# Kernel tuning notes

Measured on AMD Instinct MI355X. Metric: run time of the kernel, lower is better.

Reference implementation:

```python
import jax, jax.numpy as jnp
import numpy as np

N = 50000      # num_nodes
E = 300000     # edges per edge type
T = 3          # num_edge_type
C = 2          # num_channels
F_IN = 64      # feature_size
HID = 64       # hidden_size (w_out)
NL = 2         # num_layers (GT layers per FastGTN)
BETA = 0.5     # gtn_beta
TP = 0.8       # teleport_probability


def setup_inputs() -> dict:
    key = jax.random.key(0)
    ks = jax.random.split(key, 16)
    X = jax.random.normal(ks[0], (N, F_IN), dtype=jnp.float32)
    edge_index_0 = jax.random.randint(ks[1], (2, E), 0, N)
    edge_index_1 = jax.random.randint(ks[2], (2, E), 0, N)
    edge_index_2 = jax.random.randint(ks[3], (2, E), 0, N)
    edge_value_0 = jax.random.uniform(ks[4], (E,), dtype=jnp.float32)
    edge_value_1 = jax.random.uniform(ks[5], (E,), dtype=jnp.float32)
    edge_value_2 = jax.random.uniform(ks[6], (E,), dtype=jnp.float32)
    # glorot for Ws (per-channel projection), std=0.1 for GT layer mixing weights
    g0 = np.sqrt(6.0 / (F_IN + HID))
    g1 = np.sqrt(6.0 / (HID + HID))
    Ws0 = jax.random.uniform(ks[7], (C, F_IN, HID), minval=-g0, maxval=g0, dtype=jnp.float32)
    Ws1 = jax.random.uniform(ks[8], (C, HID, HID), minval=-g1, maxval=g1, dtype=jnp.float32)
    layerW0 = 0.1 * jax.random.normal(ks[9], (NL, C, T), dtype=jnp.float32)
    layerW1 = 0.1 * jax.random.normal(ks[10], (NL, C, T), dtype=jnp.float32)
    gl = np.sqrt(1.0 / (C * HID))
    lin_W0 = jax.random.uniform(ks[11], (C * HID, HID), minval=-gl, maxval=gl, dtype=jnp.float32)
    lin_b0 = jax.random.uniform(ks[12], (HID,), minval=-gl, maxval=gl, dtype=jnp.float32)
    lin_W1 = jax.random.uniform(ks[13], (C * HID, HID), minval=-gl, maxval=gl, dtype=jnp.float32)
    lin_b1 = jax.random.uniform(ks[14], (HID,), minval=-gl, maxval=gl, dtype=jnp.float32)
    return dict(X=X,
                edge_value_0=edge_value_0, edge_value_1=edge_value_1, edge_value_2=edge_value_2,
                Ws0=Ws0, Ws1=Ws1, layerW0=layerW0, layerW1=layerW1,
                lin_W0=lin_W0, lin_b0=lin_b0, lin_W1=lin_W1, lin_b1=lin_b1,
                edge_index_0=edge_index_0, edge_index_1=edge_index_1, edge_index_2=edge_index_2)


def _spmm_mix(H, filt, vals, etype, row, col):
    # H: [C, N, d]; filt: [C, T] softmaxed; vals: [Etot]; etype/row/col: [Etot]
    # == for each channel c: sum_j filt[c,j] * (A_j @ H[c])
    w = vals[None, :] * filt[:, etype]          # [C, Etot]
    msg = w[:, :, None] * H[:, col, :]          # [C, Etot, d]
    return jax.vmap(lambda m: jax.ops.segment_sum(m, row, num_segments=N))(msg)


def _fastgtn_block(Xin, Ws, layerW, linW, linb, row, col, vals, etype):
    H = jnp.einsum('nf,cfo->cno', Xin, Ws)      # [C, N, HID]
    X0 = jax.lax.stop_gradient(H)               # X_ = H.clone().detach()
    for l in range(NL):
        filt = jax.nn.softmax(layerW[l], axis=1)
        H = _spmm_mix(H, filt, vals, etype, row, col)
    Hm = TP * jax.nn.relu(BETA * X0 + (1.0 - BETA) * H) + (1.0 - TP) * X0
    Hm = jnp.transpose(Hm, (1, 0, 2)).reshape(N, C * Hm.shape[-1])  # [N, C*HID]
    return jax.nn.relu(Hm @ linW + linb)


def reference(X, edge_value_0, edge_value_1, edge_value_2,
              Ws0, Ws1, layerW0, layerW1,
              lin_W0, lin_b0, lin_W1, lin_b1,
              edge_index_0, edge_index_1, edge_index_2):
    row = jnp.concatenate([edge_index_0[0], edge_index_1[0], edge_index_2[0]])
    col = jnp.concatenate([edge_index_0[1], edge_index_1[1], edge_index_2[1]])
    vals = jnp.concatenate([edge_value_0, edge_value_1, edge_value_2])
    etype = jnp.repeat(jnp.arange(T), E)
    H = _fastgtn_block(X, Ws0, layerW0, lin_W0, lin_b0, row, col, vals, etype)
    H = _fastgtn_block(H, Ws1, layerW1, lin_W1, lin_b1, row, col, vals, etype)
    return H
```

## Files before the change

### kernel.cpp

```cpp
#include <hip/hip_runtime.h>
#include <hip/hip_fp16.h>

#define NN 50000
#define EE 300000
#define ETOT (3 * EE)
#define HD 64
#define RB 256
#define NB 196
#define CHUNK 8192
#define NBLKT ((EE + CHUNK - 1) / CHUNK)
#define NBT (3 * NBLKT)
#define NTOT (NB * NBT)
#define GS_VPT ((NTOT + 1023) / 1024)
#define MAXB 6144
#define PROJ_NTILE (NN / 16)
#define PP_GRID (NBT + 512)


__global__ void __launch_bounds__(256)
hist1_kernel(const int* __restrict__ ei0, const int* __restrict__ ei1,
             const int* __restrict__ ei2, int* __restrict__ hist) {
    __shared__ int lh[NB];
    int t = blockIdx.y;
    const int* ei = (t == 0) ? ei0 : (t == 1) ? ei1 : ei2;
    int tid = threadIdx.x;
    for (int i = tid; i < NB; i += 256) lh[i] = 0;
    __syncthreads();
    int e0 = blockIdx.x * CHUNK;
    for (int it = 0; it < CHUNK / 256; ++it) {
        int e = e0 + it * 256 + tid;
        if (e < EE) atomicAdd(&lh[ei[e] >> 8], 1);
    }
    __syncthreads();
    int flat = t * NBLKT + blockIdx.x;
    for (int i = tid; i < NB; i += 256) hist[flat * NB + i] = lh[i];
}

__global__ void __launch_bounds__(1024)
gscan_kernel(const int* __restrict__ hist, int* __restrict__ gbase,
             int* __restrict__ bbase, int* __restrict__ rp,
             const float* __restrict__ lw0, const float* __restrict__ lw1,
             float* __restrict__ filt) {
    __shared__ int wsum[16];
    int tid = threadIdx.x, lane = tid & 63, wv = tid >> 6;
    if (tid < 8) {
        int b = tid >> 2, l = (tid >> 1) & 1, c = tid & 1;
        const float* lw = (b == 0 ? lw0 : lw1) + l * 6 + c * 3;
        float a0 = lw[0], a1 = lw[1], a2 = lw[2];
        float m  = fmaxf(a0, fmaxf(a1, a2));
        float e0 = expf(a0 - m), e1 = expf(a1 - m), e2 = expf(a2 - m);
        float s  = e0 + e1 + e2;
        float* o = filt + tid * 3;
        o[0] = e0 / s; o[1] = e1 / s; o[2] = e2 / s;
    }
    int s0 = tid * GS_VPT;
    int local = 0;
    for (int j = 0; j < GS_VPT; ++j) {
        int s = s0 + j;
        if (s < NTOT) {
            int bucket = s / NBT, flat = s - bucket * NBT;
            local += hist[flat * NB + bucket];
        }
    }
    int x = local;
#pragma unroll
    for (int d = 1; d < 64; d <<= 1) {
        int y = __shfl_up(x, d);
        if (lane >= d) x += y;
    }
    if (lane == 63) wsum[wv] = x;
    __syncthreads();
    if (tid == 0) {
        int s = 0;
        for (int i = 0; i < 16; ++i) { int t = wsum[i]; wsum[i] = s; s += t; }
    }
    __syncthreads();
    int run = x + wsum[wv] - local;
    for (int j = 0; j < GS_VPT; ++j) {
        int s = s0 + j;
        if (s < NTOT) {
            int bucket = s / NBT, flat = s - bucket * NBT;
            gbase[flat * NB + bucket] = run;
            if (flat == 0) bbase[bucket] = run;
            run += hist[flat * NB + bucket];
        }
    }
    if (tid == 0) { bbase[NB] = ETOT; rp[NN] = ETOT; }
}

__global__ void __launch_bounds__(256)
place_proj_kernel(const int* __restrict__ ei0, const int* __restrict__ ei1,
                  const int* __restrict__ ei2,
                  const float* __restrict__ ev0, const float* __restrict__ ev1,
                  const float* __restrict__ ev2,
                  const int* __restrict__ gbase, uint2* __restrict__ staged,
                  const float* __restrict__ Xin, const float* __restrict__ Ws,
                  __half2* __restrict__ Hh) {
    __shared__ float Wl[2 * 64 * 64];
    __shared__ float Xs[16 * 65];
    __shared__ int   lbase[NB];
    int tid = threadIdx.x;

    if (blockIdx.x < NBT) {
        int flat = blockIdx.x;
        int t  = flat / NBLKT;
        int bx = flat - t * NBLKT;
        const int*   ei = (t == 0) ? ei0 : (t == 1) ? ei1 : ei2;
        const float* ev = (t == 0) ? ev0 : (t == 1) ? ev1 : ev2;
        for (int i = tid; i < NB; i += 256) lbase[i] = gbase[flat * NB + i];
        __syncthreads();
        int e0 = bx * CHUNK;
        for (int it = 0; it < CHUNK / 256; ++it) {
            int e = e0 + it * 256 + tid;
            if (e < EE) {
                int row = ei[e];
                int col = ei[EE + e];
                unsigned int q = (unsigned int)__float2int_rn(ev[e] * 16383.0f);
                unsigned int mw = (unsigned int)col | ((unsigned int)t << 16) | (q << 18);
                int pos = atomicAdd(&lbase[row >> 8], 1);
                staged[pos] = make_uint2(mw, (unsigned int)row);
            }
        }
    } else {
        for (int i = tid; i < 2 * 64 * 64; i += 256) Wl[i] = Ws[i];
        int oq = (tid & 15) * 4;
        int ln = tid >> 4;
        for (int tile = blockIdx.x - NBT; tile < PROJ_NTILE; tile += 512) {
            int n0 = tile * 16;
            __syncthreads();
            for (int i = tid; i < 16 * 64; i += 256)
                Xs[(i >> 6) * 65 + (i & 63)] = Xin[(n0 + (i >> 6)) * 64 + (i & 63)];
            __syncthreads();
            float a0[4] = {0.f, 0.f, 0.f, 0.f};
            float a1[4] = {0.f, 0.f, 0.f, 0.f};
            for (int f = 0; f < 64; ++f) {
                float  x  = Xs[ln * 65 + f];
                float4 w0 = *(const float4*)&Wl[f * 64 + oq];
                float4 w1 = *(const float4*)&Wl[4096 + f * 64 + oq];
                a0[0] += x * w0.x; a0[1] += x * w0.y;
                a0[2] += x * w0.z; a0[3] += x * w0.w;
                a1[0] += x * w1.x; a1[1] += x * w1.y;
                a1[2] += x * w1.z; a1[3] += x * w1.w;
            }
            float4 o4;
            ((__half2*)&o4)[0] = __floats2half2_rn(a0[0], a1[0]);
            ((__half2*)&o4)[1] = __floats2half2_rn(a0[1], a1[1]);
            ((__half2*)&o4)[2] = __floats2half2_rn(a0[2], a1[2]);
            ((__half2*)&o4)[3] = __floats2half2_rn(a0[3], a1[3]);
            *(float4*)&Hh[(n0 + ln) * HD + oq] = o4;
        }
    }
}

__global__ void __launch_bounds__(256)
csr_kernel(const uint2* __restrict__ staged, const int* __restrict__ bbase,
           int* __restrict__ rp, unsigned int* __restrict__ meta) {
    __shared__ int hist[RB];
    __shared__ int lcur[RB];
    __shared__ int wsum[4];
    __shared__ unsigned int metaL[MAXB];
    int b   = blockIdx.x;
    int tid = threadIdx.x;
    int base = bbase[b];
    int cnt  = bbase[b + 1] - base;
    int row0 = b * RB;

    hist[tid] = 0;
    __syncthreads();
    for (int i = tid; i < cnt; i += 256) {
        uint2 s = staged[base + i];
        atomicAdd(&hist[(int)s.y - row0], 1);
    }
    __syncthreads();
    int lane = tid & 63, wv = tid >> 6;
    int v = hist[tid];
    int x = v;
#pragma unroll
    for (int d = 1; d < 64; d <<= 1) {
        int y = __shfl_up(x, d);
        if (lane >= d) x += y;
    }
    if (lane == 63) wsum[wv] = x;
    __syncthreads();
    if (tid == 0) {
        int s = 0;
        for (int i = 0; i < 4; ++i) { int t = wsum[i]; wsum[i] = s; s += t; }
    }
    __syncthreads();
    int excl = x + wsum[wv] - v;
    lcur[tid] = excl;
    int row = row0 + tid;
    if (row < NN) rp[row] = base + excl;
    __syncthreads();
    for (int i = tid; i < cnt; i += 256) {
        uint2 s = staged[base + i];
        int p = atomicAdd(&lcur[(int)s.y - row0], 1);
        metaL[p] = s.x;
    }
    __syncthreads();
    for (int i = tid; i < cnt; i += 256)
        meta[base + i] = metaL[i];
}

__global__ void __launch_bounds__(256)
proj_kernel(const float* __restrict__ Xin, const float* __restrict__ Ws,
            __half2* __restrict__ Hh) {
    __shared__ float Wl[2 * 64 * 64];
    __shared__ float Xs[16 * 65];
    int tid = threadIdx.x;
    for (int i = tid; i < 2 * 64 * 64; i += 256) Wl[i] = Ws[i];
    int oq = (tid & 15) * 4;
    int ln = tid >> 4;
    for (int tile = blockIdx.x; tile < PROJ_NTILE; tile += gridDim.x) {
        int n0 = tile * 16;
        __syncthreads();
        for (int i = tid; i < 16 * 64; i += 256)
            Xs[(i >> 6) * 65 + (i & 63)] = Xin[(n0 + (i >> 6)) * 64 + (i & 63)];
        __syncthreads();
        float a0[4] = {0.f, 0.f, 0.f, 0.f};
        float a1[4] = {0.f, 0.f, 0.f, 0.f};
        for (int f = 0; f < 64; ++f) {
            float  x  = Xs[ln * 65 + f];
            float4 w0 = *(const float4*)&Wl[f * 64 + oq];
            float4 w1 = *(const float4*)&Wl[4096 + f * 64 + oq];
            a0[0] += x * w0.x; a0[1] += x * w0.y;
            a0[2] += x * w0.z; a0[3] += x * w0.w;
            a1[0] += x * w1.x; a1[1] += x * w1.y;
            a1[2] += x * w1.z; a1[3] += x * w1.w;
        }
        float4 o4;
        ((__half2*)&o4)[0] = __floats2half2_rn(a0[0], a1[0]);
        ((__half2*)&o4)[1] = __floats2half2_rn(a0[1], a1[1]);
        ((__half2*)&o4)[2] = __floats2half2_rn(a0[2], a1[2]);
        ((__half2*)&o4)[3] = __floats2half2_rn(a0[3], a1[3]);
        *(float4*)&Hh[(n0 + ln) * HD + oq] = o4;
    }
}

__global__ void __launch_bounds__(256)
spmm_kernel(const float4* __restrict__ Hin4, float4* __restrict__ Hout4,
            const unsigned int* __restrict__ meta, const int* __restrict__ rp,
            const float* __restrict__ filt ) {
    const int wid  = threadIdx.x >> 6;
    const int lane = threadIdx.x & 63;
    const int g    = lane >> 4;
    const int fq   = lane & 15;
    const int row  = blockIdx.x * 4 + wid;

    const float s = 1.0f / 16383.0f;
    const float F00 = filt[0] * s, F01 = filt[1] * s, F02 = filt[2] * s;
    const float F10 = filt[3] * s, F11 = filt[4] * s, F12 = filt[5] * s;

    float accA[4] = {0.f, 0.f, 0.f, 0.f};
    float accB[4] = {0.f, 0.f, 0.f, 0.f};

    const int beg = rp[row], end = rp[row + 1];
    for (int j0 = beg; j0 < end; j0 += 64) {
        int cnt = min(end - j0, 64);
        unsigned int m = (lane < cnt) ? meta[j0 + lane] : 0u;
        for (int k = 0; k < cnt; k += 8) {
            unsigned int mmA = (unsigned int)__shfl((int)m, k + g);
            unsigned int mmB = (unsigned int)__shfl((int)m, k + 4 + g);
            float4 rA = Hin4[(mmA & 0xffffu) * 16 + fq];
            float4 rB = Hin4[(mmB & 0xffffu) * 16 + fq];
            int   etA = (mmA >> 16) & 3,  etB = (mmB >> 16) & 3;
            float qA  = (float)(mmA >> 18), qB = (float)(mmB >> 18);
            float w0A = qA * ((etA == 0) ? F00 : (etA == 1) ? F01 : F02);
            float w1A = qA * ((etA == 0) ? F10 : (etA == 1) ? F11 : F12);
            float w0B = qB * ((etB == 0) ? F00 : (etB == 1) ? F01 : F02);
            float w1B = qB * ((etB == 0) ? F10 : (etB == 1) ? F11 : F12);
#pragma unroll
            for (int i = 0; i < 4; ++i) {
                float2 xA = __half22float2(((const __half2*)&rA)[i]);
                float2 xB = __half22float2(((const __half2*)&rB)[i]);
                accA[i] += w0A * xA.x + w0B * xB.x;
                accB[i] += w1A * xA.y + w1B * xB.y;
            }
        }
    }
#pragma unroll
    for (int i = 0; i < 4; ++i) {
        accA[i] += __shfl_xor(accA[i], 16); accA[i] += __shfl_xor(accA[i], 32);
        accB[i] += __shfl_xor(accB[i], 16); accB[i] += __shfl_xor(accB[i], 32);
    }
    if (g == 0) {
        float4 o4;
        ((__half2*)&o4)[0] = __floats2half2_rn(accA[0], accB[0]);
        ((__half2*)&o4)[1] = __floats2half2_rn(accA[1], accB[1]);
        ((__half2*)&o4)[2] = __floats2half2_rn(accA[2], accB[2]);
        ((__half2*)&o4)[3] = __floats2half2_rn(accA[3], accB[3]);
        Hout4[row * 16 + fq] = o4;
    }
}

#define EPI_TILE 64
#define HS_STRIDE 132
__global__ void __launch_bounds__(256)
epilogue_kernel(const __half2* __restrict__ X0, const __half2* __restrict__ H,
                const float* __restrict__ linW, const float* __restrict__ linb,
                float* __restrict__ out) {
    __shared__ float Wl[128 * 64];
    __shared__ float Hs[EPI_TILE * HS_STRIDE];
    int tid = threadIdx.x;
    for (int i = tid; i < 128 * 64; i += 256) Wl[i] = linW[i];
    int oq = tid & 15, nq = tid >> 4;
    float bias[4];
#pragma unroll
    for (int i = 0; i < 4; ++i) bias[i] = linb[oq + 16 * i];
    const int ntiles = (NN + EPI_TILE - 1) / EPI_TILE;
    for (int tile = blockIdx.x; tile < ntiles; tile += gridDim.x) {
        int n0 = tile * EPI_TILE;
        __syncthreads();
        for (int i = tid; i < EPI_TILE * 64; i += 256) {
            int ln = i >> 6, d = i & 63;
            int n = n0 + ln;
            float2 x0 = make_float2(0.f, 0.f), h = make_float2(0.f, 0.f);
            if (n < NN) {
                x0 = __half22float2(X0[n * HD + d]);
                h  = __half22float2(H [n * HD + d]);
            }
            float z0 = fmaxf(0.5f * x0.x + 0.5f * h.x, 0.f);
            float z1 = fmaxf(0.5f * x0.y + 0.5f * h.y, 0.f);
            Hs[ln * HS_STRIDE + d]      = 0.8f * z0 + 0.2f * x0.x;
            Hs[ln * HS_STRIDE + 64 + d] = 0.8f * z1 + 0.2f * x0.y;
        }
        __syncthreads();
        float acc[4][4];
#pragma unroll
        for (int j = 0; j < 4; ++j)
#pragma unroll
            for (int i = 0; i < 4; ++i) acc[j][i] = bias[i];
        for (int k = 0; k < 128; k += 4) {
            float4 hq[4];
#pragma unroll
            for (int j = 0; j < 4; ++j)
                hq[j] = *(const float4*)&Hs[(nq + 16 * j) * HS_STRIDE + k];
#pragma unroll
            for (int kk = 0; kk < 4; ++kk) {
                float w[4];
#pragma unroll
                for (int i = 0; i < 4; ++i) w[i] = Wl[(k + kk) * 64 + oq + 16 * i];
#pragma unroll
                for (int j = 0; j < 4; ++j) {
                    float x = (kk == 0) ? hq[j].x : (kk == 1) ? hq[j].y
                             : (kk == 2) ? hq[j].z : hq[j].w;
#pragma unroll
                    for (int i = 0; i < 4; ++i) acc[j][i] += x * w[i];
                }
            }
        }
#pragma unroll
        for (int j = 0; j < 4; ++j) {
            int n = n0 + nq + 16 * j;
            if (n < NN) {
#pragma unroll
                for (int i = 0; i < 4; ++i)
                    out[n * HD + oq + 16 * i] = fmaxf(acc[j][i], 0.f);
            }
        }
    }
}

extern "C" void kernel_launch(void* const* d_in, const int* in_sizes, int n_in,
                              void* d_out, int out_size, void* d_ws, size_t ws_size,
                              hipStream_t stream) {
    const float* X     = (const float*)d_in[0];
    const float* ev0   = (const float*)d_in[1];
    const float* ev1   = (const float*)d_in[2];
    const float* ev2   = (const float*)d_in[3];
    const float* Ws0   = (const float*)d_in[4];
    const float* Ws1   = (const float*)d_in[5];
    const float* lw0   = (const float*)d_in[6];
    const float* lw1   = (const float*)d_in[7];
    const float* linW0 = (const float*)d_in[8];
    const float* linb0 = (const float*)d_in[9];
    const float* linW1 = (const float*)d_in[10];
    const float* linb1 = (const float*)d_in[11];
    const int*   ei0   = (const int*)d_in[12];
    const int*   ei1   = (const int*)d_in[13];
    const int*   ei2   = (const int*)d_in[14];
    float* out = (float*)d_out;

    float* ws = (float*)d_ws;
    __half2* X0h = (__half2*)(ws);
    __half2* Ha  = (__half2*)(ws + 1 * NN * HD);
    __half2* Hb  = (__half2*)(ws + 2 * NN * HD);
    float*   mid = ws + 3 * NN * HD;
    uint2*   staged = (uint2*)mid;
    float*   filt   = ws + 4 * NN * HD;
    int*     hist   = (int*)(filt + 32);
    int*     gbase  = hist + NTOT;
    int*     bbase  = gbase + NTOT;
    int*     rp     = bbase + NB + 4;
    unsigned int* meta = (unsigned int*)(rp + NN + 16);

    dim3 egrid(NBLKT, 3);
    hist1_kernel<<<egrid, 256, 0, stream>>>(ei0, ei1, ei2, hist);
    gscan_kernel<<<1, 1024, 0, stream>>>(hist, gbase, bbase, rp,
                                         lw0, lw1, filt);
    place_proj_kernel<<<PP_GRID, 256, 0, stream>>>(ei0, ei1, ei2,
                                                   ev0, ev1, ev2,
                                                   gbase, staged,
                                                   X, Ws0, X0h);
    csr_kernel<<<NB, 256, 0, stream>>>(staged, bbase, rp, meta);

    spmm_kernel<<<NN / 4, 256, 0, stream>>>((const float4*)X0h, (float4*)Ha,
                                            meta, rp, filt + 0);
    spmm_kernel<<<NN / 4, 256, 0, stream>>>((const float4*)Ha, (float4*)Hb,
                                            meta, rp, filt + 6);
    epilogue_kernel<<<512, 256, 0, stream>>>(X0h, Hb, linW0, linb0, mid);

    proj_kernel<<<512, 256, 0, stream>>>(mid, Ws1, X0h);
    spmm_kernel<<<NN / 4, 256, 0, stream>>>((const float4*)X0h, (float4*)Ha,
                                            meta, rp, filt + 12);
    spmm_kernel<<<NN / 4, 256, 0, stream>>>((const float4*)Ha, (float4*)Hb,
                                            meta, rp, filt + 18);
    epilogue_kernel<<<512, 256, 0, stream>>>(X0h, Hb, linW1, linb1, out);
}
```

Before: 392.8 us.

## Fuse next-block projection into epilogue and unroll SpMM gather to four edges

```diff
diff --git a/kernel.cpp b/kernel.cpp
--- a/kernel.cpp
+++ b/kernel.cpp
@@ -202,38 +202,19 @@
         meta[base + i] = metaL[i];
 }
 
-__global__ void __launch_bounds__(256)
-proj_kernel(const float* __restrict__ Xin, const float* __restrict__ Ws,
-            __half2* __restrict__ Hh) {
-    __shared__ float Wl[2 * 64 * 64];
-    __shared__ float Xs[16 * 65];
-    int tid = threadIdx.x;
-    for (int i = tid; i < 2 * 64 * 64; i += 256) Wl[i] = Ws[i];
-    int oq = (tid & 15) * 4;
-    int ln = tid >> 4;
-    for (int tile = blockIdx.x; tile < PROJ_NTILE; tile += gridDim.x) {
-        int n0 = tile * 16;
-        __syncthreads();
-        for (int i = tid; i < 16 * 64; i += 256)
-            Xs[(i >> 6) * 65 + (i & 63)] = Xin[(n0 + (i >> 6)) * 64 + (i & 63)];
-        __syncthreads();
-        float a0[4] = {0.f, 0.f, 0.f, 0.f};
-        float a1[4] = {0.f, 0.f, 0.f, 0.f};
-        for (int f = 0; f < 64; ++f) {
-            float  x  = Xs[ln * 65 + f];
-            float4 w0 = *(const float4*)&Wl[f * 64 + oq];
-            float4 w1 = *(const float4*)&Wl[4096 + f * 64 + oq];
-            a0[0] += x * w0.x; a0[1] += x * w0.y;
-            a0[2] += x * w0.z; a0[3] += x * w0.w;
-            a1[0] += x * w1.x; a1[1] += x * w1.y;
-            a1[2] += x * w1.z; a1[3] += x * w1.w;
-        }
-        float4 o4;
-        ((__half2*)&o4)[0] = __floats2half2_rn(a0[0], a1[0]);
-        ((__half2*)&o4)[1] = __floats2half2_rn(a0[1], a1[1]);
-        ((__half2*)&o4)[2] = __floats2half2_rn(a0[2], a1[2]);
-        ((__half2*)&o4)[3] = __floats2half2_rn(a0[3], a1[3]);
-        *(float4*)&Hh[(n0 + ln) * HD + oq] = o4;
+__device__ __forceinline__ void edge_acc(unsigned int mm, float4 r,
+                                         float F00, float F01, float F02,
+                                         float F10, float F11, float F12,
+                                         float* accA, float* accB) {
+    int   et = (mm >> 16) & 3;
+    float q  = (float)(mm >> 18);
+    float w0 = q * ((et == 0) ? F00 : (et == 1) ? F01 : F02);
+    float w1 = q * ((et == 0) ? F10 : (et == 1) ? F11 : F12);
+#pragma unroll
+    for (int i = 0; i < 4; ++i) {
+        float2 x = __half22float2(((const __half2*)&r)[i]);
+        accA[i] += w0 * x.x;
+        accB[i] += w1 * x.y;
     }
 }
 
@@ -258,23 +239,27 @@
     for (int j0 = beg; j0 < end; j0 += 64) {
         int cnt = min(end - j0, 64);
         unsigned int m = (lane < cnt) ? meta[j0 + lane] : 0u;
-        for (int k = 0; k < cnt; k += 8) {
-            unsigned int mmA = (unsigned int)__shfl((int)m, k + g);
-            unsigned int mmB = (unsigned int)__shfl((int)m, k + 4 + g);
-            float4 rA = Hin4[(mmA & 0xffffu) * 16 + fq];
-            float4 rB = Hin4[(mmB & 0xffffu) * 16 + fq];
-            int   etA = (mmA >> 16) & 3,  etB = (mmB >> 16) & 3;
-            float qA  = (float)(mmA >> 18), qB = (float)(mmB >> 18);
-            float w0A = qA * ((etA == 0) ? F00 : (etA == 1) ? F01 : F02);
-            float w1A = qA * ((etA == 0) ? F10 : (etA == 1) ? F11 : F12);
-            float w0B = qB * ((etB == 0) ? F00 : (etB == 1) ? F01 : F02);
-            float w1B = qB * ((etB == 0) ? F10 : (etB == 1) ? F11 : F12);
-#pragma unroll
-            for (int i = 0; i < 4; ++i) {
-                float2 xA = __half22float2(((const __half2*)&rA)[i]);
-                float2 xB = __half22float2(((const __half2*)&rB)[i]);
-                accA[i] += w0A * xA.x + w0B * xB.x;
-                accB[i] += w1A * xA.y + w1B * xB.y;
+        for (int k = 0; k < cnt; k += 16) {
+            if (k + 8 < cnt) {
+                unsigned int mmA = (unsigned int)__shfl((int)m, k + g);
+                unsigned int mmB = (unsigned int)__shfl((int)m, k + 4 + g);
+                unsigned int mmC = (unsigned int)__shfl((int)m, k + 8 + g);
+                unsigned int mmD = (unsigned int)__shfl((int)m, k + 12 + g);
+                float4 rA = Hin4[(mmA & 0xffffu) * 16 + fq];
+                float4 rB = Hin4[(mmB & 0xffffu) * 16 + fq];
+                float4 rC = Hin4[(mmC & 0xffffu) * 16 + fq];
+                float4 rD = Hin4[(mmD & 0xffffu) * 16 + fq];
+                edge_acc(mmA, rA, F00, F01, F02, F10, F11, F12, accA, accB);
+                edge_acc(mmB, rB, F00, F01, F02, F10, F11, F12, accA, accB);
+                edge_acc(mmC, rC, F00, F01, F02, F10, F11, F12, accA, accB);
+                edge_acc(mmD, rD, F00, F01, F02, F10, F11, F12, accA, accB);
+            } else {
+                unsigned int mmA = (unsigned int)__shfl((int)m, k + g);
+                unsigned int mmB = (unsigned int)__shfl((int)m, k + 4 + g);
+                float4 rA = Hin4[(mmA & 0xffffu) * 16 + fq];
+                float4 rB = Hin4[(mmB & 0xffffu) * 16 + fq];
+                edge_acc(mmA, rA, F00, F01, F02, F10, F11, F12, accA, accB);
+                edge_acc(mmB, rB, F00, F01, F02, F10, F11, F12, accA, accB);
             }
         }
     }
@@ -295,10 +280,12 @@
 
 #define EPI_TILE 64
 #define HS_STRIDE 132
+template<bool PROJ>
 __global__ void __launch_bounds__(256)
 epilogue_kernel(const __half2* __restrict__ X0, const __half2* __restrict__ H,
                 const float* __restrict__ linW, const float* __restrict__ linb,
-                float* __restrict__ out) {
+                const float* __restrict__ Wsn, float* __restrict__ out,
+                __half2* __restrict__ X0out) {
     __shared__ float Wl[128 * 64];
     __shared__ float Hs[EPI_TILE * HS_STRIDE];
     int tid = threadIdx.x;
@@ -349,13 +336,55 @@
                 }
             }
         }
-#pragma unroll
-        for (int j = 0; j < 4; ++j) {
-            int n = n0 + nq + 16 * j;
-            if (n < NN) {
+        if (!PROJ) {
+#pragma unroll
+            for (int j = 0; j < 4; ++j) {
+                int n = n0 + nq + 16 * j;
+                if (n < NN) {
+#pragma unroll
+                    for (int i = 0; i < 4; ++i)
+                        out[n * HD + oq + 16 * i] = fmaxf(acc[j][i], 0.f);
+                }
+            }
+        } else {
+            __syncthreads();
+#pragma unroll
+            for (int j = 0; j < 4; ++j)
 #pragma unroll
                 for (int i = 0; i < 4; ++i)
-                    out[n * HD + oq + 16 * i] = fmaxf(acc[j][i], 0.f);
+                    Hs[(nq + 16 * j) * HS_STRIDE + oq + 16 * i] =
+                        fmaxf(acc[j][i], 0.f);
+            __syncthreads();
+            int ln2 = tid >> 4;
+            int oq2 = (tid & 15) * 4;
+            float p0[4][4], p1[4][4];
+#pragma unroll
+            for (int j = 0; j < 4; ++j)
+#pragma unroll
+                for (int i = 0; i < 4; ++i) { p0[j][i] = 0.f; p1[j][i] = 0.f; }
+            for (int f = 0; f < 64; ++f) {
+                float4 w0 = *(const float4*)&Wsn[f * 64 + oq2];
+                float4 w1 = *(const float4*)&Wsn[4096 + f * 64 + oq2];
+#pragma unroll
+                for (int j = 0; j < 4; ++j) {
+                    float x = Hs[(j * 16 + ln2) * HS_STRIDE + f];
+                    p0[j][0] += x * w0.x; p0[j][1] += x * w0.y;
+                    p0[j][2] += x * w0.z; p0[j][3] += x * w0.w;
+                    p1[j][0] += x * w1.x; p1[j][1] += x * w1.y;
+                    p1[j][2] += x * w1.z; p1[j][3] += x * w1.w;
+                }
+            }
+#pragma unroll
+            for (int j = 0; j < 4; ++j) {
+                int n = n0 + j * 16 + ln2;
+                if (n < NN) {
+                    float4 o4;
+                    ((__half2*)&o4)[0] = __floats2half2_rn(p0[j][0], p1[j][0]);
+                    ((__half2*)&o4)[1] = __floats2half2_rn(p0[j][1], p1[j][1]);
+                    ((__half2*)&o4)[2] = __floats2half2_rn(p0[j][2], p1[j][2]);
+                    ((__half2*)&o4)[3] = __floats2half2_rn(p0[j][3], p1[j][3]);
+                    *(float4*)&X0out[n * HD + oq2] = o4;
+                }
             }
         }
     }
@@ -385,8 +414,7 @@
     __half2* X0h = (__half2*)(ws);
     __half2* Ha  = (__half2*)(ws + 1 * NN * HD);
     __half2* Hb  = (__half2*)(ws + 2 * NN * HD);
-    float*   mid = ws + 3 * NN * HD;
-    uint2*   staged = (uint2*)mid;
+    uint2*   staged = (uint2*)(ws + 3 * NN * HD);
     float*   filt   = ws + 4 * NN * HD;
     int*     hist   = (int*)(filt + 32);
     int*     gbase  = hist + NTOT;
@@ -408,12 +436,13 @@
                                             meta, rp, filt + 0);
     spmm_kernel<<<NN / 4, 256, 0, stream>>>((const float4*)Ha, (float4*)Hb,
                                             meta, rp, filt + 6);
-    epilogue_kernel<<<512, 256, 0, stream>>>(X0h, Hb, linW0, linb0, mid);
-
-    proj_kernel<<<512, 256, 0, stream>>>(mid, Ws1, X0h);
+    epilogue_kernel<true><<<784, 256, 0, stream>>>(X0h, Hb, linW0, linb0,
+                                                   Ws1, nullptr, X0h);
+
     spmm_kernel<<<NN / 4, 256, 0, stream>>>((const float4*)X0h, (float4*)Ha,
                                             meta, rp, filt + 12);
     spmm_kernel<<<NN / 4, 256, 0, stream>>>((const float4*)Ha, (float4*)Hb,
                                             meta, rp, filt + 18);
-    epilogue_kernel<<<512, 256, 0, stream>>>(X0h, Hb, linW1, linb1, out);
-}
+    epilogue_kernel<false><<<784, 256, 0, stream>>>(X0h, Hb, linW1, linb1,
+                                                    Ws1, out, nullptr);
+}
```

Measured after the change: 385.5 us, median of 2. Within noise of the previous version (-1.9%).
